# Kernel tuning notes

Measured on AMD Instinct MI355X. Metric: run time of the kernel, lower is better.

## Reference

```python
import jax, jax.numpy as jnp
import numpy as np

M = 4  # mixture size of the AttentionStem value embedding

def unfold_windows(a, kh, kw, Hout, Wout):
    # a: [..., Hp, Wp] -> [..., Hout, Wout, kh, kw] (stride-1 sliding windows, cropped)
    rows = []
    for i in range(kh):
        cols = [a[..., i:i + Hout, j:j + Wout] for j in range(kw)]
        rows.append(jnp.stack(cols, axis=-1))
    return jnp.stack(rows, axis=-2)

def attention_stem(x, qw, kw_, vw, emb_a, emb_b, emb_mix, kh, kw, pad):
    # x: [B,Cin,H,W]; qw/kw_: [Cin,Co]; vw: [M,Cin,Co]; emb_a:[Co,kh]; emb_b:[Co,kw]; emb_mix:[M,Co]
    B, Cin, H, W = x.shape
    pl, pr, pt, pb = pad  # F.pad order (left,right,top,bottom)
    xp = jnp.pad(x, ((0, 0), (0, 0), (pt, pb), (pl, pr)))
    Hp, Wp = xp.shape[2], xp.shape[3]
    Hout = min(Hp - kh + 1, H)
    Wout = min(Wp - kw + 1, W)
    q = jnp.einsum('bchw,co->bohw', x[:, :, :Hout, :Wout], qw)       # 1x1 conv query
    k = jnp.einsum('bchw,co->bohw', xp, kw_)                          # 1x1 conv key on padded
    v = jnp.einsum('bchw,mco->mbohw', xp, vw)                         # m 1x1 conv values
    k_win = unfold_windows(k, kh, kw, Hout, Wout)                     # [B,Co,Ho,Wo,kh,kw]
    v_win = unfold_windows(v, kh, kw, Hout, Wout)                     # [M,B,Co,Ho,Wo,kh,kw]
    # mixture relative-position embedding, softmax over mixtures per (kh,kw) offset
    la = emb_mix @ emb_a                                              # [M,kh]
    lb = emb_mix @ emb_b                                              # [M,kw]
    emb = jax.nn.softmax(la[:, :, None] + lb[:, None, :], axis=0)     # [M,kh,kw]
    v_agg = jnp.einsum('mkl,mbohwkl->bohwkl', emb, v_win)             # [B,Co,Ho,Wo,kh,kw]
    K = kh * kw
    scores = jnp.einsum('bohw,bohwkl->bhwkl', q, k_win).reshape(B, Hout, Wout, K)
    attn = jax.nn.softmax(scores, axis=-1).reshape(B, Hout, Wout, kh, kw)
    out = jnp.einsum('bhwkl,bohwkl->bohw', attn, v_agg)               # [B,Co,Ho,Wo]
    return out

def bn_relu(x, g, b):
    # training-mode BatchNorm2d + ReLU
    mu = x.mean(axis=(0, 2, 3), keepdims=True)
    var = x.var(axis=(0, 2, 3), keepdims=True)
    y = (x - mu) * jax.lax.rsqrt(var + 1e-5) * g[None, :, None, None] + b[None, :, None, None]
    return jax.nn.relu(y)

def _params(key):
    ks = jax.random.split(key, 18)
    def w(k, shape):
        return jax.random.normal(k, shape, dtype=jnp.float32) * 0.1
    cfg = [(1, 64, 1, 5), (64, 128, 2, 5), (128, 16, 2, 5)]
    p = {}
    i = 0
    for s, (ci, co, kh, kw) in enumerate(cfg):
        p[f'p{s}_q'] = w(ks[i], (ci, co)); i += 1
        p[f'p{s}_k'] = w(ks[i], (ci, co)); i += 1
        p[f'p{s}_v'] = w(ks[i], (M, ci, co)); i += 1
        p[f'p{s}_ea'] = w(ks[i], (co, kh)); i += 1
        p[f'p{s}_eb'] = w(ks[i], (co, kw)); i += 1
        p[f'p{s}_em'] = w(ks[i], (M, co)); i += 1
        p[f'p{s}_g'] = jnp.ones((co,), jnp.float32)
        p[f'p{s}_b'] = jnp.zeros((co,), jnp.float32)
    return p

def setup_inputs() -> dict:
    key = jax.random.key(0)
    kx, kp = jax.random.split(key)
    inp = {'x': jax.random.normal(kx, (2, 1, 8, 3000), dtype=jnp.float32)}
    inp.update(_params(kp))
    return inp

def reference(x,
              p0_q, p0_k, p0_v, p0_ea, p0_eb, p0_em, p0_g, p0_b,
              p1_q, p1_k, p1_v, p1_ea, p1_eb, p1_em, p1_g, p1_b,
              p2_q, p2_k, p2_v, p2_ea, p2_eb, p2_em, p2_g, p2_b):
    h = attention_stem(x, p0_q, p0_k, p0_v, p0_ea, p0_eb, p0_em, 1, 5, (2, 2, 0, 0))
    h = bn_relu(h, p0_g, p0_b)[:, :, ::2, ::2]                        # MaxPool2d(1,2) == stride-2 subsample
    h = attention_stem(h, p1_q, p1_k, p1_v, p1_ea, p1_eb, p1_em, 2, 5, (2, 2, 1, 1))
    h = bn_relu(h, p1_g, p1_b)[:, :, ::2, ::2]
    h = attention_stem(h, p2_q, p2_k, p2_v, p2_ea, p2_eb, p2_em, 2, 5, (2, 2, 0, 0))
    h = bn_relu(h, p2_g, p2_b)
    B, C, H, W = h.shape
    nW = W // 56                                                       # AvgPool2d((1,56))
    return h[:, :, :, :nW * 56].reshape(B, C, H, nW, 56).mean(-1)
```

## Files before the change

### kernel.cpp

```cpp
#include <hip/hip_runtime.h>
#include <math.h>


#define TPB 256

__global__ void prep0_kernel(const float* __restrict__ ea,
                             const float* __restrict__ eb,
                             const float* __restrict__ em,
                             const float* __restrict__ qw,
                             const float* __restrict__ kw_,
                             const float* __restrict__ vw,
                             float* __restrict__ par) {
    const int M4 = 4, Co = 64, kw = 5;
    __shared__ float la[4];
    __shared__ float lb[20];
    __shared__ float embs[20];
    int tid = threadIdx.x;
    if (tid < 64) {
        float p = qw[tid] * kw_[tid];
#pragma unroll
        for (int d = 1; d < 64; d <<= 1) p += __shfl_xor(p, d, 64);
        if (tid == 0) par[0] = p;
    }
    if (tid >= 64 && tid < 64 + M4) {
        int m = tid - 64;
        float s = 0.f;
        for (int o = 0; o < Co; ++o) s += em[m * Co + o] * ea[o];
        la[m] = s;
    }
    if (tid >= 128 && tid < 128 + M4 * kw) {
        int r = tid - 128;
        int m = r / kw, l = r % kw;
        float s = 0.f;
        for (int o = 0; o < Co; ++o) s += em[m * Co + o] * eb[o * kw + l];
        lb[m * kw + l] = s;
    }
    __syncthreads();
    if (tid < 5) {
        float lg[4];
        float mx = -1e30f;
        for (int m = 0; m < M4; ++m) {
            lg[m] = la[m] + lb[m * kw + tid];
            mx = fmaxf(mx, lg[m]);
        }
        float sum = 0.f;
        for (int m = 0; m < M4; ++m) { lg[m] = expf(lg[m] - mx); sum += lg[m]; }
        float inv = 1.f / sum;
        for (int m = 0; m < M4; ++m) embs[tid * 4 + m] = lg[m] * inv;
    }
    __syncthreads();
    for (int e = tid; e < 5 * 64; e += blockDim.x) {
        int t = e / 64, o = e - t * 64;
        float s = 0.f;
        for (int m = 0; m < M4; ++m) s += embs[t * 4 + m] * vw[m * 64 + o];
        par[1 + e] = s;
    }
}

__global__ void attn_out0_kernel(const float* __restrict__ x,
                                 const float* __restrict__ par,
                                 float* __restrict__ h0raw,
                                 float2* __restrict__ part0) {
    __shared__ float wsh[5][256];
    __shared__ float vsh[5 * 64];
    __shared__ float wred[4][20];
    __shared__ float wfin[20];
    int tid = threadIdx.x;
    int b = blockIdx.y;
    int oz = blockIdx.z;
    int n0 = blockIdx.x * 256;
    int n = n0 + tid;
    for (int i = tid; i < 320; i += 256) vsh[i] = par[1 + i];
    float c0 = par[0];
    float warr[5];
    if (n < 24000) {
        int h = n / 3000, w = n - h * 3000;
        const float* xr = x + b * 24000 + h * 3000;
        float xc = xr[w];
        float xs[5], s[5];
#pragma unroll
        for (int t = 0; t < 5; ++t) {
            int col = w + t - 2;
            xs[t] = (col >= 0 && col < 3000) ? xr[col] : 0.f;
            s[t] = c0 * xc * xs[t];
        }
        float mx = s[0];
#pragma unroll
        for (int t = 1; t < 5; ++t) mx = fmaxf(mx, s[t]);
        float sum = 0.f;
#pragma unroll
        for (int t = 0; t < 5; ++t) { s[t] = expf(s[t] - mx); sum += s[t]; }
        float inv = 1.f / sum;
#pragma unroll
        for (int t = 0; t < 5; ++t) warr[t] = s[t] * inv * xs[t];
    } else {
#pragma unroll
        for (int t = 0; t < 5; ++t) warr[t] = 0.f;
    }
#pragma unroll
    for (int t = 0; t < 5; ++t) wsh[t][tid] = warr[t];
    float p[20];
#pragma unroll
    for (int t = 0; t < 5; ++t) p[t] = warr[t];
    {
        int k = 5;
#pragma unroll
        for (int t = 0; t < 5; ++t)
#pragma unroll
            for (int t2 = t; t2 < 5; ++t2) p[k++] = warr[t] * warr[t2];
    }
#pragma unroll
    for (int d = 1; d < 64; d <<= 1)
#pragma unroll
        for (int i = 0; i < 20; ++i) p[i] += __shfl_xor(p[i], d, 64);
    if ((tid & 63) == 0)
#pragma unroll
        for (int i = 0; i < 20; ++i) wred[tid >> 6][i] = p[i];
    __syncthreads();
    if (tid < 20)
        wfin[tid] = wred[0][tid] + wred[1][tid] + wred[2][tid] + wred[3][tid];
    __syncthreads();
    int jq = tid & 63, og = tid >> 6;
    int nq = n0 + jq * 4;
    int h = nq / 3000, w0 = nq - h * 3000;
    bool st = (nq < 24000) && ((h & 1) == 0);
    float wq[5][4];
#pragma unroll
    for (int t = 0; t < 5; ++t)
#pragma unroll
        for (int j = 0; j < 4; ++j) wq[t][j] = wsh[t][jq * 4 + j];
    int obase = oz * 32 + og * 8;
    for (int oi = 0; oi < 8; ++oi) {
        int o = obase + oi;
        float4 v = make_float4(0.f, 0.f, 0.f, 0.f);
#pragma unroll
        for (int t = 0; t < 5; ++t) {
            float vo = vsh[t * 64 + o];
            v.x = fmaf(wq[t][0], vo, v.x);
            v.y = fmaf(wq[t][1], vo, v.y);
            v.z = fmaf(wq[t][2], vo, v.z);
            v.w = fmaf(wq[t][3], vo, v.w);
        }
        if (st) {
            size_t base = ((size_t)b * 64 + o) * 6000 + (h >> 1) * 1500 + (w0 >> 1);
            *(float2*)&h0raw[base] = make_float2(v.x, v.z);
        }
    }
    if (tid < 32) {
        int o = oz * 32 + tid;
        float vt[5];
#pragma unroll
        for (int t = 0; t < 5; ++t) vt[t] = vsh[t * 64 + o];
        float s = 0.f, s2 = 0.f;
#pragma unroll
        for (int t = 0; t < 5; ++t) s = fmaf(vt[t], wfin[t], s);
        int k = 5;
#pragma unroll
        for (int t = 0; t < 5; ++t)
#pragma unroll
            for (int t2 = t; t2 < 5; ++t2) {
                float coef = (t == t2) ? vt[t] * vt[t] : 2.f * vt[t] * vt[t2];
                s2 = fmaf(coef, wfin[k], s2);
                ++k;
            }
        int chunk = b * gridDim.x + blockIdx.x;
        part0[(size_t)o * 188 + chunk] = make_float2(s, s2);
    }
}

__global__ void prep_stage1_kernel(const float* __restrict__ ea,
                                   const float* __restrict__ eb,
                                   const float* __restrict__ em,
                                   const float* __restrict__ qw,
                                   const float* __restrict__ kw_,
                                   const float* __restrict__ vw,
                                   float* __restrict__ G,
                                   float* __restrict__ Av,
                                   const float2* __restrict__ part0,
                                   float* __restrict__ mr0) {
    const int M4 = 4, Co = 128, kh = 2, kw = 5, Cin = 64;
    __shared__ float la[8];
    __shared__ float lb[20];
    __shared__ float embs[40];
    int tid = threadIdx.x;
    if (blockIdx.x == 0 && tid < 64) {
        double s = 0.0, s2 = 0.0;
        for (int i = 0; i < 188; ++i) {
            float2 p = part0[(size_t)tid * 188 + i];
            s += p.x; s2 += p.y;
        }
        double mean = s / 48000.0;
        double var = s2 / 48000.0 - mean * mean;
        mr0[tid] = (float)mean;
        mr0[64 + tid] = (float)(1.0 / sqrt(var + 1e-5));
    }
    if (tid < M4 * kh) {
        int m = tid / kh, k = tid % kh;
        float s = 0.f;
        for (int o = 0; o < Co; ++o) s += em[m * Co + o] * ea[o * kh + k];
        la[tid] = s;
    }
    if (tid >= 64 && tid < 64 + M4 * kw) {
        int r = tid - 64;
        int m = r / kw, l = r % kw;
        float s = 0.f;
        for (int o = 0; o < Co; ++o) s += em[m * Co + o] * eb[o * kw + l];
        lb[r] = s;
    }
    __syncthreads();
    if (tid < 10) {
        int k = tid / kw, l = tid % kw;
        float lg[4];
        float mx = -1e30f;
        for (int m = 0; m < M4; ++m) {
            lg[m] = la[m * kh + k] + lb[m * kw + l];
            mx = fmaxf(mx, lg[m]);
        }
        float sum = 0.f;
        for (int m = 0; m < M4; ++m) { lg[m] = expf(lg[m] - mx); sum += lg[m]; }
        float inv = 1.f / sum;
        for (int m = 0; m < M4; ++m) embs[tid * 4 + m] = lg[m] * inv;
    }
    __syncthreads();
    const int TOTG = 64 * 64;
    const int TOT2 = 640 * 128;
    int nth = gridDim.x * blockDim.x;
    for (int e = blockIdx.x * blockDim.x + tid; e < TOTG + TOT2; e += nth) {
        if (e < TOTG) {
            int c = e >> 6, c2 = e & 63;
            float s = 0.f;
            for (int o = 0; o < 128; ++o)
                s = fmaf(qw[c * 128 + o], kw_[c2 * 128 + o], s);
            G[e] = s;
        } else {
            int e2 = e - TOTG;
            int k = e2 / Co, o = e2 - k * Co;
            int c = k / 10, t = k - c * 10;
            float val = 0.f;
            for (int m = 0; m < M4; ++m)
                val += embs[t * 4 + m] * vw[(m * Cin + c) * Co + o];
            Av[e2] = val;
        }
    }
}

__global__ void prep_wcat_kernel(const float* __restrict__ ea,
                                 const float* __restrict__ eb,
                                 const float* __restrict__ em,
                                 const float* __restrict__ qw,
                                 const float* __restrict__ kw_,
                                 const float* __restrict__ vw,
                                 float* __restrict__ Wcat,
                                 int Co, int kh, int kw, int Cin,
                                 const float2* __restrict__ part,
                                 float* __restrict__ mr,
                                 int Cprev, int NCH, int count) {
    const int M4 = 4;
    __shared__ float la[8];
    __shared__ float lb[20];
    __shared__ float embs[40];
    int K = kh * kw;
    int tid = threadIdx.x;
    if (blockIdx.x == 0 && tid < Cprev) {
        double s = 0.0, s2 = 0.0;
        for (int i = 0; i < NCH; ++i) {
            float2 p = part[(size_t)tid * NCH + i];
            s += p.x; s2 += p.y;
        }
        double mean = s / count;
        double var = s2 / count - mean * mean;
        mr[tid] = (float)mean;
        mr[Cprev + tid] = (float)(1.0 / sqrt(var + 1e-5));
    }
    if (tid < M4 * kh) {
        int m = tid / kh, k = tid % kh;
        float s = 0.f;
        for (int o = 0; o < Co; ++o) s += em[m * Co + o] * ea[o * kh + k];
        la[tid] = s;
    }
    if (tid >= 64 && tid < 64 + M4 * kw) {
        int r = tid - 64;
        int m = r / kw, l = r % kw;
        float s = 0.f;
        for (int o = 0; o < Co; ++o) s += em[m * Co + o] * eb[o * kw + l];
        lb[r] = s;
    }
    __syncthreads();
    if (tid < K) {
        int k = tid / kw, l = tid % kw;
        float lg[4];
        float mx = -1e30f;
        for (int m = 0; m < M4; ++m) {
            lg[m] = la[m * kh + k] + lb[m * kw + l];
            mx = fmaxf(mx, lg[m]);
        }
        float sum = 0.f;
        for (int m = 0; m < M4; ++m) { lg[m] = expf(lg[m] - mx); sum += lg[m]; }
        float inv = 1.f / sum;
        for (int m = 0; m < M4; ++m) embs[tid * 4 + m] = lg[m] * inv;
    }
    __syncthreads();
    int Mtot = (2 + K) * Co;
    long long total = (long long)Mtot * Cin;
    for (long long e = (long long)blockIdx.x * blockDim.x + tid; e < total;
         e += (long long)gridDim.x * blockDim.x) {
        int m = (int)(e / Cin);
        int c = (int)(e - (long long)m * Cin);
        float val;
        if (m < Co) {
            val = qw[c * Co + m];
        } else if (m < 2 * Co) {
            val = kw_[c * Co + (m - Co)];
        } else {
            int mz = m - 2 * Co;
            int t = mz / Co;
            int o = mz - t * Co;
            val = 0.f;
            for (int mm = 0; mm < M4; ++mm)
                val += embs[t * 4 + mm] * vw[(mm * Cin + c) * Co + o];
        }
        Wcat[e] = val;
    }
}

__global__ void attn_v4_kernel(const float* __restrict__ G,
                               const float* __restrict__ xraw,
                               const float* __restrict__ mr,
                               const float* __restrict__ g,
                               const float* __restrict__ bb,
                               float* __restrict__ attn) {
    __shared__ float xw[64][2][68];
    __shared__ float gbuf[64][64];
    __shared__ float ssh[64][12];
    __shared__ float scb[64], sfb[64];
    int tid = threadIdx.x;
    int chunk = blockIdx.x;
    int ho = blockIdx.y;
    int b = blockIdx.z;
    int wo0 = chunk * 64;
    if (tid < 64) {
        float sc = mr[64 + tid] * g[tid];
        scb[tid] = sc;
        sfb[tid] = bb[tid] - mr[tid] * sc;
    }
    for (int e = tid; e < 4096; e += 256)
        gbuf[e >> 6][e & 63] = G[e];
    __syncthreads();
    for (int e = tid; e < 64 * 136; e += 256) {
        int c = e / 136;
        int r2 = e - c * 136;
        int r = r2 / 68, jj = r2 - r * 68;
        int row = ho - 1 + r;
        int col = wo0 + jj - 2;
        float v = 0.f;
        if (row >= 0 && col >= 0 && col < 1500) {
            float xv = xraw[((size_t)b * 64 + c) * 6000 + row * 1500 + col];
            v = fmaxf(fmaf(xv, scb[c], sfb[c]), 0.f);
        }
        xw[c][r][jj] = v;
    }
    __syncthreads();
    int j = tid & 63, cg = tid >> 6;
    float ul[16];
#pragma unroll
    for (int i = 0; i < 16; ++i) ul[i] = 0.f;
    for (int c = 0; c < 64; ++c) {
        float xv = xw[c][1][j + 2];
#pragma unroll
        for (int i = 0; i < 16; ++i)
            ul[i] = fmaf(gbuf[c][cg * 16 + i], xv, ul[i]);
    }
    __syncthreads();
#pragma unroll
    for (int i = 0; i < 16; ++i) gbuf[cg * 16 + i][j] = ul[i];
    __syncthreads();
    int t0 = cg, t1 = cg + 4, t2 = cg + 8;
    int dk0 = t0 / 5, dl0 = t0 % 5;
    int dk1 = t1 / 5, dl1 = t1 % 5;
    int dk2 = (t2 < 10) ? 1 : 0, dl2 = (t2 < 10) ? (t2 - 5) : 0;
    float s0 = 0.f, s1 = 0.f, s2v = 0.f;
    for (int c = 0; c < 64; ++c) {
        float uv = gbuf[c][j];
        s0 = fmaf(uv, xw[c][dk0][j + dl0], s0);
        s1 = fmaf(uv, xw[c][dk1][j + dl1], s1);
        if (t2 < 10) s2v = fmaf(uv, xw[c][dk2][j + dl2], s2v);
    }
    ssh[j][t0] = s0;
    ssh[j][t1] = s1;
    if (t2 < 10) ssh[j][t2] = s2v;
    __syncthreads();
    if (tid < 64 && wo0 + tid < 1500) {
        float sc[10];
        float mx = -1e30f;
#pragma unroll
        for (int t = 0; t < 10; ++t) { sc[t] = ssh[tid][t]; mx = fmaxf(mx, sc[t]); }
        float sum = 0.f;
#pragma unroll
        for (int t = 0; t < 10; ++t) { sc[t] = expf(sc[t] - mx); sum += sc[t]; }
        float inv = 1.f / sum;
        int n = ho * 1500 + wo0 + tid;
#pragma unroll
        for (int t = 0; t < 10; ++t)
            attn[((size_t)b * 10 + t) * 6000 + n] = sc[t] * inv;
    }
}

__launch_bounds__(256)
__global__ void vgemm_kernel(const float* __restrict__ Av,
                             const float* __restrict__ xraw,
                             const float* __restrict__ attn,
                             const float* __restrict__ mr,
                             const float* __restrict__ g,
                             const float* __restrict__ bb,
                             float* __restrict__ partial) {
    __shared__ float As[40][68];
    __shared__ float Bs[40][68];
    __shared__ float xw[32][2][68];
    __shared__ float att_s[10][64];
    __shared__ float scl[32], sfl[32];
    int tid = threadIdx.x;
    int nt = blockIdx.x;
    int ho = nt / 24, chunk = nt - ho * 24;
    int wo0 = chunk * 64;
    int my = blockIdx.y;
    int mt = my >> 1, sk = my & 1;
    int m0 = mt * 64;
    int b = blockIdx.z;
    int c_base = sk * 32;
    if (tid < 32) {
        int c = c_base + tid;
        float sc = mr[64 + c] * g[c];
        scl[tid] = sc;
        sfl[tid] = bb[c] - mr[c] * sc;
    }
    __syncthreads();
    for (int e = tid; e < 32 * 136; e += 256) {
        int c = e / 136;
        int r2 = e - c * 136;
        int r = r2 / 68, jj = r2 - r * 68;
        int row = ho - 1 + r;
        int col = wo0 + jj - 2;
        float v = 0.f;
        if (row >= 0 && col >= 0 && col < 1500) {
            float xv = xraw[((size_t)b * 64 + c_base + c) * 6000 + row * 1500 + col];
            v = fmaxf(fmaf(xv, scl[c], sfl[c]), 0.f);
        }
        xw[c][r][jj] = v;
    }
    for (int e = tid; e < 640; e += 256) {
        int t = e >> 6, jj = e & 63;
        int col = wo0 + jj;
        att_s[t][jj] = (col < 1500)
            ? attn[((size_t)b * 10 + t) * 6000 + ho * 1500 + col] : 0.f;
    }
    __syncthreads();
    float acc[4][4] = {{0.f}};
    int tm = tid & 15, tn = tid >> 4;
    int arow = c_base * 10;
    for (int k0 = 0; k0 < 320; k0 += 40) {
#pragma unroll
        for (int it = 0; it < 10; ++it) {
            int e = it * 256 + tid;
            int kk = e >> 6, mm = e & 63;
            As[kk][mm] = Av[(size_t)(arow + k0 + kk) * 128 + m0 + mm];
        }
#pragma unroll
        for (int it = 0; it < 10; ++it) {
            int e = it * 256 + tid;
            int kk = e >> 6, jj = e & 63;
            int kg = k0 + kk;
            int cl = kg / 10, t = kg - cl * 10;
            int dk = t / 5, dl = t - dk * 5;
            Bs[kk][jj] = xw[cl][dk][jj + dl] * att_s[t][jj];
        }
        __syncthreads();
#pragma unroll 8
        for (int k = 0; k < 40; ++k) {
            float4 a4 = *(const float4*)&As[k][tm * 4];
            float4 b4 = *(const float4*)&Bs[k][tn * 4];
            float av[4] = {a4.x, a4.y, a4.z, a4.w};
            float bv[4] = {b4.x, b4.y, b4.z, b4.w};
#pragma unroll
            for (int i = 0; i < 4; ++i)
#pragma unroll
                for (int jx = 0; jx < 4; ++jx)
                    acc[i][jx] = fmaf(av[i], bv[jx], acc[i][jx]);
        }
        __syncthreads();
    }
    int wo = wo0 + tn * 4;
    if (wo < 1500) {
        int n = ho * 1500 + wo;
#pragma unroll
        for (int i = 0; i < 4; ++i) {
            int o = m0 + tm * 4 + i;
            float* pp = &partial[(((size_t)sk * 2 + b) * 128 + o) * 6000 + n];
            *(float4*)pp = make_float4(acc[i][0], acc[i][1], acc[i][2], acc[i][3]);
        }
    }
}

__global__ void vreduce_kernel(const float* __restrict__ partial,
                               float* __restrict__ h1raw,
                               float2* __restrict__ part1) {
    int tid = threadIdx.x;
    int by = blockIdx.y;
    int b = by >> 7, o = by & 127;
    int n = blockIdx.x * 1024 + tid * 4;
    float4 v = make_float4(0.f, 0.f, 0.f, 0.f);
    if (n < 6000) {
#pragma unroll
        for (int sk = 0; sk < 2; ++sk) {
            float4 p = *(const float4*)&partial[(((size_t)sk * 2 + b) * 128 + o) * 6000 + n];
            v.x += p.x; v.y += p.y; v.z += p.z; v.w += p.w;
        }
        int ho = n / 1500, wo = n - ho * 1500;
        if ((ho & 1) == 0) {
            size_t base = ((size_t)b * 128 + o) * 1500 + (ho >> 1) * 750 + (wo >> 1);
            *(float2*)&h1raw[base] = make_float2(v.x, v.z);
        }
    }
    float s = v.x + v.y + v.z + v.w;
    float s2 = v.x * v.x + v.y * v.y + v.z * v.z + v.w * v.w;
    __shared__ float sh[TPB], sh2[TPB];
    sh[tid] = s; sh2[tid] = s2;
    __syncthreads();
    for (int st = TPB / 2; st > 0; st >>= 1) {
        if (tid < st) { sh[tid] += sh[tid + st]; sh2[tid] += sh2[tid + st]; }
        __syncthreads();
    }
    if (tid == 0)
        part1[(size_t)o * 12 + b * 6 + blockIdx.x] = make_float2(sh[0], sh2[0]);
}

__launch_bounds__(256, 4)
__global__ void gemm_qkbn_kernel(const float* __restrict__ A,
                                 const float* __restrict__ xraw,
                                 const float* __restrict__ mr,
                                 const float* __restrict__ g,
                                 const float* __restrict__ bb,
                                 float* __restrict__ qk,
                                 float* __restrict__ z,
                                 int M, int N, int K, int twoCo) {
    __shared__ float As[32][132];
    __shared__ float Bs[32][132];
    __shared__ float scale[128], shift[128];
    int tid = threadIdx.x;
    int b = blockIdx.z;
    int m0 = blockIdx.y * 128, n0 = blockIdx.x * 128;
    int Mz = M - twoCo;
    float acc[8][8] = {{0.f}};
    int am = tid >> 1, ak = (tid & 1) * 16;
    int bk = tid >> 3, bn = (tid & 7) * 16;
    int tm = tid & 15, tn = tid >> 4;
    for (int c = tid; c < K; c += 256) {
        float sc = mr[K + c] * g[c];
        scale[c] = sc;
        shift[c] = bb[c] - mr[c] * sc;
    }
    __syncthreads();
    for (int k0 = 0; k0 < K; k0 += 32) {
        {
            int mA = m0 + am;
            const float* Ap = A + (size_t)mA * K + k0 + ak;
#pragma unroll
            for (int q = 0; q < 4; ++q) {
                float4 v = (mA < M) ? *(const float4*)(Ap + q * 4)
                                    : make_float4(0.f, 0.f, 0.f, 0.f);
                int kk = ak + q * 4;
                As[kk + 0][am] = v.x;
                As[kk + 1][am] = v.y;
                As[kk + 2][am] = v.z;
                As[kk + 3][am] = v.w;
            }
        }
        {
            int c = k0 + bk;
            float sc = scale[c], sf = shift[c];
            const float* Xp = xraw + ((size_t)b * K + c) * N + n0 + bn;
            if (n0 + 128 <= N) {
#pragma unroll
                for (int q = 0; q < 4; ++q) {
                    float4 v = *(const float4*)(Xp + q * 4);
                    v.x = fmaxf(fmaf(v.x, sc, sf), 0.f);
                    v.y = fmaxf(fmaf(v.y, sc, sf), 0.f);
                    v.z = fmaxf(fmaf(v.z, sc, sf), 0.f);
                    v.w = fmaxf(fmaf(v.w, sc, sf), 0.f);
                    *(float4*)&Bs[bk][bn + q * 4] = v;
                }
            } else {
#pragma unroll
                for (int q = 0; q < 16; ++q) {
                    int n = n0 + bn + q;
                    Bs[bk][bn + q] = (n < N) ? fmaxf(fmaf(Xp[q], sc, sf), 0.f) : 0.f;
                }
            }
        }
        __syncthreads();
#pragma unroll 8
        for (int k = 0; k < 32; ++k) {
            float4 a0 = *(const float4*)&As[k][tm * 4];
            float4 a1 = *(const float4*)&As[k][64 + tm * 4];
            float4 b0 = *(const float4*)&Bs[k][tn * 4];
            float4 b1 = *(const float4*)&Bs[k][64 + tn * 4];
            float av[8] = {a0.x, a0.y, a0.z, a0.w, a1.x, a1.y, a1.z, a1.w};
            float bv[8] = {b0.x, b0.y, b0.z, b0.w, b1.x, b1.y, b1.z, b1.w};
#pragma unroll
            for (int i = 0; i < 8; ++i)
#pragma unroll
                for (int j = 0; j < 8; ++j)
                    acc[i][j] = fmaf(av[i], bv[j], acc[i][j]);
        }
        __syncthreads();
    }
    bool fullN = (n0 + 128 <= N);
#pragma unroll
    for (int iq = 0; iq < 2; ++iq) {
        int mb = m0 + iq * 64 + tm * 4;
        if (mb >= M) continue;
        if (mb < twoCo) {
#pragma unroll
            for (int jq = 0; jq < 2; ++jq)
#pragma unroll
                for (int jj = 0; jj < 4; ++jj) {
                    int n = n0 + jq * 64 + tn * 4 + jj;
                    if (n < N) {
                        float4 v = make_float4(acc[iq * 4 + 0][jq * 4 + jj],
                                               acc[iq * 4 + 1][jq * 4 + jj],
                                               acc[iq * 4 + 2][jq * 4 + jj],
                                               acc[iq * 4 + 3][jq * 4 + jj]);
                        *(float4*)&qk[((size_t)b * N + n) * twoCo + mb] = v;
                    }
                }
        } else {
#pragma unroll
            for (int i = 0; i < 4; ++i) {
                int row = mb + i - twoCo;
                float* zp = &z[((size_t)b * Mz + row) * N];
#pragma unroll
                for (int jq = 0; jq < 2; ++jq) {
                    int nb_ = n0 + jq * 64 + tn * 4;
                    if (fullN) {
                        *(float4*)&zp[nb_] = make_float4(acc[iq * 4 + i][jq * 4 + 0],
                                                         acc[iq * 4 + i][jq * 4 + 1],
                                                         acc[iq * 4 + i][jq * 4 + 2],
                                                         acc[iq * 4 + i][jq * 4 + 3]);
                    } else {
#pragma unroll
                        for (int jj = 0; jj < 4; ++jj)
                            if (nb_ + jj < N) zp[nb_ + jj] = acc[iq * 4 + i][jq * 4 + jj];
                    }
                }
            }
        }
    }
}

template <int KH, int KW, int CO, int NPB>
__global__ void attn_v3_kernel(const float* __restrict__ qk,
                               float* __restrict__ attn,
                               int H, int W, int Ho, int Wo, int pt, int pl) {
    const int K = KH * KW;
    __shared__ float ssh[NPB][K];
    int tid = threadIdx.x;
    int b = blockIdx.y;
    int ln = tid / K, t = tid - ln * K;
    int Nout = Ho * Wo;
    int n = blockIdx.x * NPB + ln;
    bool active = (tid < NPB * K) && (n < Nout);
    int HWin = H * W;
    float sv = 0.f;
    if (active) {
        int ho = n / Wo, wo = n - ho * Wo;
        int row = ho + t / KW - pt, col = wo + t % KW - pl;
        if (row >= 0 && row < H && col >= 0 && col < W) {
            const float* qp = qk + ((size_t)b * HWin + ho * W + wo) * (2 * CO);
            const float* kp = qk + ((size_t)b * HWin + (size_t)row * W + col) * (2 * CO) + CO;
#pragma unroll
            for (int o = 0; o < CO; o += 4) {
                float4 q4 = *(const float4*)(qp + o);
                float4 k4 = *(const float4*)(kp + o);
                sv += q4.x * k4.x + q4.y * k4.y + q4.z * k4.z + q4.w * k4.w;
            }
        }
        ssh[ln][t] = sv;
    }
    __syncthreads();
    if (active) {
        float mx = ssh[ln][0];
#pragma unroll
        for (int tt = 1; tt < K; ++tt) mx = fmaxf(mx, ssh[ln][tt]);
        float sum = 0.f;
#pragma unroll
        for (int tt = 0; tt < K; ++tt) sum += expf(ssh[ln][tt] - mx);
        float num = expf(sv - mx);
        attn[((size_t)b * K + t) * Nout + n] = num / sum;
    }
}

template <int KH, int KW>
__global__ void combine_stats_kernel(const float* __restrict__ z,
                                     const float* __restrict__ attn,
                                     float* __restrict__ out,
                                     float2* __restrict__ part,
                                     int Co, int Mz,
                                     int H, int W, int Ho, int Wo,
                                     int pt, int pl) {
    const int K = KH * KW;
    int tid = threadIdx.x;
    int bc = blockIdx.y;
    int b = bc / Co, o = bc - b * Co;
    int Nout = Ho * Wo, Nin = H * W;
    int n = blockIdx.x * blockDim.x + tid;
    float val = 0.f;
    if (n < Nout) {
        int ho = n / Wo, wo = n - ho * Wo;
#pragma unroll
        for (int dk = 0; dk < KH; ++dk) {
            int row = ho + dk - pt;
            if (row < 0 || row >= H) continue;
#pragma unroll
            for (int dl = 0; dl < KW; ++dl) {
                int col = wo + dl - pl;
                if (col < 0 || col >= W) continue;
                int t = dk * KW + dl;
                float a = attn[((size_t)b * K + t) * Nout + n];
                float zv = z[((size_t)b * Mz + t * Co + o) * Nin + row * W + col];
                val = fmaf(a, zv, val);
            }
        }
        out[((size_t)b * Co + o) * Nout + n] = val;
    }
    __shared__ float sh[TPB], sh2[TPB];
    sh[tid] = (n < Nout) ? val : 0.f;
    sh2[tid] = (n < Nout) ? val * val : 0.f;
    __syncthreads();
    for (int st = TPB / 2; st > 0; st >>= 1) {
        if (tid < st) { sh[tid] += sh[tid + st]; sh2[tid] += sh2[tid + st]; }
        __syncthreads();
    }
    if (tid == 0) {
        int chunk = b * gridDim.x + blockIdx.x;
        part[(size_t)o * (2 * gridDim.x) + chunk] = make_float2(sh[0], sh2[0]);
    }
}

__global__ void bn_avg_final_kernel(const float* __restrict__ x,
                                    const float2* __restrict__ part,
                                    const float* __restrict__ g,
                                    const float* __restrict__ bb,
                                    float* __restrict__ out,
                                    int B, int C, int W, int nW, int NCH) {
    int idx = blockIdx.x * blockDim.x + threadIdx.x;
    int N = B * C * nW;
    if (idx >= N) return;
    int j = idx % nW; int r = idx / nW;
    int c = r % C; int b = r / C;
    double s = 0.0, s2 = 0.0;
    for (int i = 0; i < NCH; ++i) {
        float2 p = part[(size_t)c * NCH + i];
        s += p.x; s2 += p.y;
    }
    double cnt = (double)B * W;
    double mean = s / cnt;
    double var = s2 / cnt - mean * mean;
    float rstd = (float)(1.0 / sqrt(var + 1e-5));
    float meanf = (float)mean, gg = g[c], bo = bb[c];
    const float* xb = x + ((long long)b * C + c) * W + j * 56;
    float acc = 0.f;
    for (int i = 0; i < 56; ++i) {
        float yn = (xb[i] - meanf) * rstd * gg + bo;
        acc += fmaxf(yn, 0.f);
    }
    out[idx] = acc * (1.f / 56.f);
}

extern "C" void kernel_launch(void* const* d_in, const int* in_sizes, int n_in,
                              void* d_out, int out_size, void* d_ws, size_t ws_size,
                              hipStream_t stream) {
    const float* x   = (const float*)d_in[0];
    const float* qw0 = (const float*)d_in[1];
    const float* kw0 = (const float*)d_in[2];
    const float* vw0 = (const float*)d_in[3];
    const float* ea0 = (const float*)d_in[4];
    const float* eb0 = (const float*)d_in[5];
    const float* em0 = (const float*)d_in[6];
    const float* g0  = (const float*)d_in[7];
    const float* b0  = (const float*)d_in[8];
    const float* qw1 = (const float*)d_in[9];
    const float* kw1 = (const float*)d_in[10];
    const float* vw1 = (const float*)d_in[11];
    const float* ea1 = (const float*)d_in[12];
    const float* eb1 = (const float*)d_in[13];
    const float* em1 = (const float*)d_in[14];
    const float* g1  = (const float*)d_in[15];
    const float* b1  = (const float*)d_in[16];
    const float* qw2 = (const float*)d_in[17];
    const float* kw2 = (const float*)d_in[18];
    const float* vw2 = (const float*)d_in[19];
    const float* ea2 = (const float*)d_in[20];
    const float* eb2 = (const float*)d_in[21];
    const float* em2 = (const float*)d_in[22];
    const float* g2  = (const float*)d_in[23];
    const float* b2  = (const float*)d_in[24];
    float* outp = (float*)d_out;
    (void)ws_size; (void)in_sizes; (void)n_in; (void)out_size;

    float* ws = (float*)d_ws;
    size_t off = 0;
    auto alloc = [&](size_t n) { float* p = ws + off; off += (n + 63) & ~(size_t)63; return p; };

    float* par0   = alloc(321);
    float* part0  = alloc(64 * 188 * 2);
    float* mr0    = alloc(128);
    float* h0raw  = alloc(2 * 64 * 6000);
    float* G1     = alloc(64 * 64);
    float* Av1    = alloc(640 * 128);
    float* attn1  = alloc(2 * 10 * 6000);
    float* vpart  = alloc(2 * 2 * 128 * 6000);
    float* part1  = alloc(128 * 12 * 2);
    float* mr1    = alloc(256);
    float* h1raw  = alloc(2 * 128 * 1500);
    float* Wcat2  = alloc(192 * 128);
    float* qk2    = alloc(2 * 1500 * 32);
    float* z2     = alloc(2 * 160 * 1500);
    float* attn2  = alloc(2 * 10 * 750);
    float* part2  = alloc(16 * 6 * 2);
    float* s2     = alloc(2 * 16 * 750);

    auto grid = [](int n) { return (n + TPB - 1) / TPB; };

    prep0_kernel<<<1, TPB, 0, stream>>>(ea0, eb0, em0, qw0, kw0, vw0, par0);
    {
        dim3 g(94, 2, 2);
        attn_out0_kernel<<<g, TPB, 0, stream>>>(x, par0, h0raw, (float2*)part0);
    }
    prep_stage1_kernel<<<64, TPB, 0, stream>>>(ea1, eb1, em1, qw1, kw1, vw1,
        G1, Av1, (const float2*)part0, mr0);
    {
        dim3 g(24, 4, 2);
        attn_v4_kernel<<<g, TPB, 0, stream>>>(G1, h0raw, mr0, g0, b0, attn1);
    }
    {
        dim3 g(96, 4, 2);
        vgemm_kernel<<<g, TPB, 0, stream>>>(Av1, h0raw, attn1, mr0, g0, b0, vpart);
    }
    {
        dim3 g(6, 256);
        vreduce_kernel<<<g, TPB, 0, stream>>>(vpart, h1raw, (float2*)part1);
    }
    prep_wcat_kernel<<<24, TPB, 0, stream>>>(ea2, eb2, em2, qw2, kw2, vw2, Wcat2,
        16, 2, 5, 128, (const float2*)part1, mr1, 128, 12, 12000);
    {
        dim3 g(12, 2, 2);
        gemm_qkbn_kernel<<<g, TPB, 0, stream>>>(Wcat2, h1raw, mr1, g1, b1,
            qk2, z2, 192, 1500, 128, 32);
    }
    {
        dim3 g(750 / 25, 2);
        attn_v3_kernel<2, 5, 16, 25><<<g, TPB, 0, stream>>>(qk2, attn2,
            2, 750, 1, 750, 0, 2);
    }
    {
        dim3 g(3, 2 * 16);
        combine_stats_kernel<2, 5><<<g, TPB, 0, stream>>>(z2, attn2, s2,
            (float2*)part2, 16, 160, 2, 750, 1, 750, 0, 2);
    }
    bn_avg_final_kernel<<<grid(2 * 16 * 13), TPB, 0, stream>>>(s2, (const float2*)part2,
        g2, b2, outp, 2, 16, 750, 13, 6);
}
```

Before: 259.2 us.

## Restructure stage-1 value GEMM to read wave-uniform weights directly and split-K by four

The value GEMM kernel no longer stages the A (Av) tile in shared memory. Each wave instead covers 32 output channels, reading them through a wave-uniform pointer so the compiler can use scalar loads, while each lane owns one output column and keeps 32 accumulators. The K dimension is split into four channel groups instead of two, so the partial buffer doubles and the reduce kernel sums four slices. A separate small edit in the score kernel vectorises the gbuf reads with float4. The trade is more partial-sum memory traffic and more register pressure in exchange for less shared-memory traffic and fewer barriers.

New measurement: 257.5 us (median of 2 runs). No clear change (-0.7%).

```diff
diff --git a/kernel.cpp b/kernel.cpp
--- a/kernel.cpp
+++ b/kernel.cpp
@@ -366,9 +366,18 @@
     for (int i = 0; i < 16; ++i) ul[i] = 0.f;
     for (int c = 0; c < 64; ++c) {
         float xv = xw[c][1][j + 2];
-#pragma unroll
-        for (int i = 0; i < 16; ++i)
-            ul[i] = fmaf(gbuf[c][cg * 16 + i], xv, ul[i]);
+        float4 g0 = *(const float4*)&gbuf[c][cg * 16 + 0];
+        float4 g1 = *(const float4*)&gbuf[c][cg * 16 + 4];
+        float4 g2 = *(const float4*)&gbuf[c][cg * 16 + 8];
+        float4 g3 = *(const float4*)&gbuf[c][cg * 16 + 12];
+        ul[0]  = fmaf(g0.x, xv, ul[0]);  ul[1]  = fmaf(g0.y, xv, ul[1]);
+        ul[2]  = fmaf(g0.z, xv, ul[2]);  ul[3]  = fmaf(g0.w, xv, ul[3]);
+        ul[4]  = fmaf(g1.x, xv, ul[4]);  ul[5]  = fmaf(g1.y, xv, ul[5]);
+        ul[6]  = fmaf(g1.z, xv, ul[6]);  ul[7]  = fmaf(g1.w, xv, ul[7]);
+        ul[8]  = fmaf(g2.x, xv, ul[8]);  ul[9]  = fmaf(g2.y, xv, ul[9]);
+        ul[10] = fmaf(g2.z, xv, ul[10]); ul[11] = fmaf(g2.w, xv, ul[11]);
+        ul[12] = fmaf(g3.x, xv, ul[12]); ul[13] = fmaf(g3.y, xv, ul[13]);
+        ul[14] = fmaf(g3.z, xv, ul[14]); ul[15] = fmaf(g3.w, xv, ul[15]);
     }
     __syncthreads();
 #pragma unroll
@@ -413,28 +422,28 @@
                              const float* __restrict__ g,
                              const float* __restrict__ bb,
                              float* __restrict__ partial) {
-    __shared__ float As[40][68];
-    __shared__ float Bs[40][68];
-    __shared__ float xw[32][2][68];
+    __shared__ float Bs[20][64];
+    __shared__ float xw[16][2][68];
     __shared__ float att_s[10][64];
-    __shared__ float scl[32], sfl[32];
+    __shared__ float scl[16], sfl[16];
     int tid = threadIdx.x;
     int nt = blockIdx.x;
     int ho = nt / 24, chunk = nt - ho * 24;
     int wo0 = chunk * 64;
-    int my = blockIdx.y;
-    int mt = my >> 1, sk = my & 1;
-    int m0 = mt * 64;
+    int sk = blockIdx.y;
     int b = blockIdx.z;
-    int c_base = sk * 32;
-    if (tid < 32) {
+    int c_base = sk * 16;
+    int lane = tid & 63;
+    int wq = tid >> 6;
+    int wqu = __builtin_amdgcn_readfirstlane(wq);
+    if (tid < 16) {
         int c = c_base + tid;
         float sc = mr[64 + c] * g[c];
         scl[tid] = sc;
         sfl[tid] = bb[c] - mr[c] * sc;
     }
     __syncthreads();
-    for (int e = tid; e < 32 * 136; e += 256) {
+    for (int e = tid; e < 16 * 136; e += 256) {
         int c = e / 136;
         int r2 = e - c * 136;
         int r = r2 / 68, jj = r2 - r * 68;
@@ -454,48 +463,35 @@
             ? attn[((size_t)b * 10 + t) * 6000 + ho * 1500 + col] : 0.f;
     }
     __syncthreads();
-    float acc[4][4] = {{0.f}};
-    int tm = tid & 15, tn = tid >> 4;
-    int arow = c_base * 10;
-    for (int k0 = 0; k0 < 320; k0 += 40) {
-#pragma unroll
-        for (int it = 0; it < 10; ++it) {
-            int e = it * 256 + tid;
-            int kk = e >> 6, mm = e & 63;
-            As[kk][mm] = Av[(size_t)(arow + k0 + kk) * 128 + m0 + mm];
-        }
-#pragma unroll
-        for (int it = 0; it < 10; ++it) {
-            int e = it * 256 + tid;
-            int kk = e >> 6, jj = e & 63;
-            int kg = k0 + kk;
-            int cl = kg / 10, t = kg - cl * 10;
-            int dk = t / 5, dl = t - dk * 5;
-            Bs[kk][jj] = xw[cl][dk][jj + dl] * att_s[t][jj];
-        }
+    float acc[32];
+#pragma unroll
+    for (int i = 0; i < 32; ++i) acc[i] = 0.f;
+    int dk = wq & 1;
+    int clh = wq >> 1;
+    for (int kc = 0; kc < 8; ++kc) {
+#pragma unroll
+        for (int it = 0; it < 5; ++it)
+            Bs[wq * 5 + it][lane] =
+                xw[kc * 2 + clh][dk][lane + it] * att_s[dk * 5 + it][lane];
         __syncthreads();
-#pragma unroll 8
-        for (int k = 0; k < 40; ++k) {
-            float4 a4 = *(const float4*)&As[k][tm * 4];
-            float4 b4 = *(const float4*)&Bs[k][tn * 4];
-            float av[4] = {a4.x, a4.y, a4.z, a4.w};
-            float bv[4] = {b4.x, b4.y, b4.z, b4.w};
-#pragma unroll
-            for (int i = 0; i < 4; ++i)
-#pragma unroll
-                for (int jx = 0; jx < 4; ++jx)
-                    acc[i][jx] = fmaf(av[i], bv[jx], acc[i][jx]);
+        const float* ap0 = Av + (size_t)(c_base * 10 + kc * 20) * 128 + wqu * 32;
+#pragma unroll
+        for (int kk = 0; kk < 20; ++kk) {
+            float bv = Bs[kk][lane];
+            const float* ap = ap0 + kk * 128;
+#pragma unroll
+            for (int i = 0; i < 32; ++i)
+                acc[i] = fmaf(ap[i], bv, acc[i]);
         }
         __syncthreads();
     }
-    int wo = wo0 + tn * 4;
+    int wo = wo0 + lane;
     if (wo < 1500) {
         int n = ho * 1500 + wo;
 #pragma unroll
-        for (int i = 0; i < 4; ++i) {
-            int o = m0 + tm * 4 + i;
-            float* pp = &partial[(((size_t)sk * 2 + b) * 128 + o) * 6000 + n];
-            *(float4*)pp = make_float4(acc[i][0], acc[i][1], acc[i][2], acc[i][3]);
+        for (int i = 0; i < 32; ++i) {
+            int o = wq * 32 + i;
+            partial[(((size_t)sk * 2 + b) * 128 + o) * 6000 + n] = acc[i];
         }
     }
 }
@@ -510,7 +506,7 @@
     float4 v = make_float4(0.f, 0.f, 0.f, 0.f);
     if (n < 6000) {
 #pragma unroll
-        for (int sk = 0; sk < 2; ++sk) {
+        for (int sk = 0; sk < 4; ++sk) {
             float4 p = *(const float4*)&partial[(((size_t)sk * 2 + b) * 128 + o) * 6000 + n];
             v.x += p.x; v.y += p.y; v.z += p.z; v.w += p.w;
         }
@@ -817,7 +813,7 @@
     float* G1     = alloc(64 * 64);
     float* Av1    = alloc(640 * 128);
     float* attn1  = alloc(2 * 10 * 6000);
-    float* vpart  = alloc(2 * 2 * 128 * 6000);
+    float* vpart  = alloc(4 * 2 * 128 * 6000);
     float* part1  = alloc(128 * 12 * 2);
     float* mr1    = alloc(256);
     float* h1raw  = alloc(2 * 128 * 1500);
```
